# Kernel tuning notes

Hardware: AMD Instinct MI355X
Metric: run time of the kernel (lower is better)

The kernel has to match this reference:

```python
import jax, jax.numpy as jnp
import numpy as np

OUT_FEATURES = 11008  # LLaMA-7B FFN intermediate
IN_FEATURES = 4096    # d_model
N_TOKENS = 16         # small M -> weight-traffic bound
SCALE = 0.01
ZERO_POINT = 0


def setup_inputs() -> dict:
    key = jax.random.key(0)
    k1, k2 = jax.random.split(key)
    x = jax.random.normal(k1, (N_TOKENS, IN_FEATURES), dtype=jnp.float32)
    weight_int8 = jax.random.randint(
        k2, (OUT_FEATURES, IN_FEATURES), -128, 128, dtype=jnp.int32
    ).astype(jnp.int8)
    return {
        "x": x,
        "weight_int8": weight_int8,
        "scale": SCALE,
        "zero_point": ZERO_POINT,
    }


def reference(x, weight_int8, scale, zero_point):
    # Dequantize INT8 weight to fp32 (same elementwise pass as the torch module)
    weight_fp = (weight_int8.astype(jnp.float32) - zero_point) * scale  # [out, in]
    # F.linear(x, W) == x @ W.T
    return jnp.einsum("ti,oi->to", x, weight_fp)
```

## Files before the change

kernel.cpp:

```cpp
#include <hip/hip_runtime.h>
#include <hip/hip_bf16.h>
#include <stdint.h>


#define M_TOK 16
#define K_DIM 4096
#define N_OUT 11008

typedef int v4i __attribute__((ext_vector_type(4)));

__global__ __launch_bounds__(256) void quant_x_kernel(
    const float* __restrict__ x, int8_t* __restrict__ xh,
    int8_t* __restrict__ xl, float* __restrict__ s1_out,
    float* __restrict__ sumx_out) {
  const int t = blockIdx.x;
  const int tid = threadIdx.x;
  const float4* xv = (const float4*)(x + (long)t * K_DIM) + tid * 4;

  float vals[16];
  float m = 0.0f, s = 0.0f;
#pragma unroll
  for (int j = 0; j < 4; ++j) {
    float4 f = xv[j];
    vals[j * 4 + 0] = f.x; vals[j * 4 + 1] = f.y;
    vals[j * 4 + 2] = f.z; vals[j * 4 + 3] = f.w;
    m = fmaxf(m, fmaxf(fmaxf(fabsf(f.x), fabsf(f.y)),
                       fmaxf(fabsf(f.z), fabsf(f.w))));
    s += f.x + f.y + f.z + f.w;
  }
#pragma unroll
  for (int off = 32; off > 0; off >>= 1) {
    m = fmaxf(m, __shfl_xor(m, off));
    s += __shfl_xor(s, off);
  }
  __shared__ float lm[4], ls[4];
  const int w = tid >> 6;
  if ((tid & 63) == 0) { lm[w] = m; ls[w] = s; }
  __syncthreads();
  m = fmaxf(fmaxf(lm[0], lm[1]), fmaxf(lm[2], lm[3]));
  s = ls[0] + ls[1] + ls[2] + ls[3];

  const float s1 = (m > 0.0f) ? (m * (1.0f / 127.0f)) : 1.0f;
  const float inv = 1.0f / s1;
  if (tid == 0) { s1_out[t] = s1; sumx_out[t] = s; }

  int hq[16], lq[16];
#pragma unroll
  for (int j = 0; j < 16; ++j) {
    float xf = vals[j];
    float h = rintf(xf * inv);
    h = fminf(fmaxf(h, -127.0f), 127.0f);
    float resid = xf - h * s1;
    float l = rintf(resid * inv * 256.0f);
    l = fminf(fmaxf(l, -128.0f), 127.0f);
    hq[j] = (int)h;
    lq[j] = (int)l;
  }
  int4 hv, lv;
  int* hp = (int*)&hv;
  int* lp = (int*)&lv;
#pragma unroll
  for (int d = 0; d < 4; ++d) {
    uint32_t hw = 0, lw = 0;
#pragma unroll
    for (int j = 0; j < 4; ++j) {
      hw |= (uint32_t)(hq[d * 4 + j] & 0xff) << (8 * j);
      lw |= (uint32_t)(lq[d * 4 + j] & 0xff) << (8 * j);
    }
    hp[d] = (int)hw;
    lp[d] = (int)lw;
  }
  ((int4*)xh)[(long)t * 256 + tid] = hv;
  ((int4*)xl)[(long)t * 256 + tid] = lv;
}

__global__ __launch_bounds__(256) void qgemm_kernel(
    const int* __restrict__ W, const int8_t* __restrict__ xh,
    const int8_t* __restrict__ xl, const float* __restrict__ s1,
    const float* __restrict__ sumx, const float* __restrict__ scale_p,
    const int* __restrict__ zp_p, float* __restrict__ out) {
  const int tid = threadIdx.x;
  const int lane = tid & 63;
  const int w = tid >> 6;
  const int obase = blockIdx.x * 16;
  const int n = lane & 15;
  const int g = lane >> 4;
  const long kbase = (long)w * 1024 + g * 16;

  const int* Wp = W + (long)(obase + n) * K_DIM + kbase;
  const v4i* Ah = (const v4i*)(xh + (long)n * K_DIM + kbase);
  const v4i* Al = (const v4i*)(xl + (long)n * K_DIM + kbase);

  v4i accH = {0, 0, 0, 0};
  v4i accL = {0, 0, 0, 0};
#pragma unroll 4
  for (int c = 0; c < 16; ++c) {
    const int4* wq = (const int4*)(Wp + c * 64);
    v4i b;
#pragma unroll
    for (int d = 0; d < 4; ++d) {
      int4 q = wq[d];
      uint32_t packed = ((uint32_t)q.x & 0xffu) |
                        (((uint32_t)q.y & 0xffu) << 8) |
                        (((uint32_t)q.z & 0xffu) << 16) |
                        (((uint32_t)q.w & 0xffu) << 24);
      b[d] = (int)packed;
    }
    v4i ah = Ah[c * 4];
    v4i al = Al[c * 4];
    accH = __builtin_amdgcn_mfma_i32_16x16x64_i8(ah, b, accH, 0, 0, 0);
    accL = __builtin_amdgcn_mfma_i32_16x16x64_i8(al, b, accL, 0, 0, 0);
  }

  __shared__ float red[4][16 * 17];
#pragma unroll
  for (int r = 0; r < 4; ++r) {
    float f = (float)accH[r] + (float)accL[r] * (1.0f / 256.0f);
    int t = g * 4 + r;
    red[w][t * 17 + n] = f;
  }
  __syncthreads();

  const int t = tid >> 4;
  const int col = tid & 15;
  float sum = red[0][t * 17 + col] + red[1][t * 17 + col] +
              red[2][t * 17 + col] + red[3][t * 17 + col];
  const float sc = scale_p[0];
  const float zp = (float)zp_p[0];
  float o = sc * (s1[t] * sum) - sc * zp * sumx[t];
  out[(long)t * N_OUT + obase + col] = o;
}

extern "C" void kernel_launch(void* const* d_in, const int* in_sizes, int n_in,
                              void* d_out, int out_size, void* d_ws,
                              size_t ws_size, hipStream_t stream) {
  const float* x = (const float*)d_in[0];
  const int* Wq = (const int*)d_in[1];
  const float* scale_p = (const float*)d_in[2];
  const int* zp_p = (const int*)d_in[3];
  float* out = (float*)d_out;

  int8_t* xh = (int8_t*)d_ws;
  int8_t* xl = xh + (long)M_TOK * K_DIM;
  float* s1 = (float*)(xl + (long)M_TOK * K_DIM);
  float* sumx = s1 + M_TOK;

  quant_x_kernel<<<M_TOK, 256, 0, stream>>>(x, xh, xl, s1, sumx);
  qgemm_kernel<<<N_OUT / 16, 256, 0, stream>>>(Wq, xh, xl, s1, sumx, scale_p,
                                               zp_p, out);
}
```

Baseline: 255.1 us.

## Double-buffer weight tiles via async global-to-LDS loads with swizzled layout

The GEMM kernel now streams weight tiles into shared memory with `global_load_lds` DMA, double-buffered so the next stage's load is in flight while MFMAs run on the current one. The K split across waves is reorganised so each wave owns 64-int slices per stage. Lanes now read 256 contiguous bytes per row instead of 64, which should coalesce better. An XOR swizzle is meant to avoid LDS bank conflicts on readback. The code relies on the compiler inserting vmcnt waits before the LDS reads and adds no explicit barrier, which is a correctness risk; LDS use also grows, which may lower occupancy.

```diff
diff --git a/kernel.cpp b/kernel.cpp
--- a/kernel.cpp
+++ b/kernel.cpp
@@ -8,6 +8,11 @@
 #define N_OUT 11008
 
 typedef int v4i __attribute__((ext_vector_type(4)));
+
+#define GLOAD_LDS16(g, l)                                               \
+  __builtin_amdgcn_global_load_lds(                                     \
+      (const __attribute__((address_space(1))) void*)(g),               \
+      (__attribute__((address_space(3))) void*)(l), 16, 0, 0)
 
 __global__ __launch_bounds__(256) void quant_x_kernel(
     const float* __restrict__ x, int8_t* __restrict__ xh,
@@ -85,31 +90,61 @@
   const int obase = blockIdx.x * 16;
   const int n = lane & 15;
   const int g = lane >> 4;
-  const long kbase = (long)w * 1024 + g * 16;
 
-  const int* Wp = W + (long)(obase + n) * K_DIM + kbase;
-  const v4i* Ah = (const v4i*)(xh + (long)n * K_DIM + kbase);
-  const v4i* Al = (const v4i*)(xl + (long)n * K_DIM + kbase);
+  __shared__ int wlds[2][4][1024];
+
+  const int* gj0 = W + (long)(obase + 0 + g) * K_DIM + w * 64 + ((n ^ g) ^ 0) * 4;
+  const int* gj1 = W + (long)(obase + 4 + g) * K_DIM + w * 64 + ((n ^ g) ^ 4) * 4;
+  const int* gj2 = W + (long)(obase + 8 + g) * K_DIM + w * 64 + ((n ^ g) ^ 0) * 4;
+  const int* gj3 = W + (long)(obase + 12 + g) * K_DIM + w * 64 + ((n ^ g) ^ 4) * 4;
+
+  const int Q0 = (g * 4) ^ (n & 7);
+  const int r0 = n * 64 + ((Q0 ^ 0)) * 4;
+  const int r1 = n * 64 + ((Q0 ^ 1)) * 4;
+  const int r2 = n * 64 + ((Q0 ^ 2)) * 4;
+  const int r3 = n * 64 + ((Q0 ^ 3)) * 4;
+
+  const v4i* Ah = (const v4i*)(xh + (long)n * K_DIM + w * 64 + g * 16);
+  const v4i* Al = (const v4i*)(xl + (long)n * K_DIM + w * 64 + g * 16);
 
   v4i accH = {0, 0, 0, 0};
   v4i accL = {0, 0, 0, 0};
-#pragma unroll 4
-  for (int c = 0; c < 16; ++c) {
-    const int4* wq = (const int4*)(Wp + c * 64);
-    v4i b;
+
+  GLOAD_LDS16(gj0, &wlds[0][w][0]);
+  GLOAD_LDS16(gj1, &wlds[0][w][256]);
+  GLOAD_LDS16(gj2, &wlds[0][w][512]);
+  GLOAD_LDS16(gj3, &wlds[0][w][768]);
+
 #pragma unroll
-    for (int d = 0; d < 4; ++d) {
-      int4 q = wq[d];
-      uint32_t packed = ((uint32_t)q.x & 0xffu) |
-                        (((uint32_t)q.y & 0xffu) << 8) |
-                        (((uint32_t)q.z & 0xffu) << 16) |
-                        (((uint32_t)q.w & 0xffu) << 24);
-      b[d] = (int)packed;
+  for (int s = 0; s < 16; ++s) {
+    const int b = s & 1;
+    if (s + 1 < 16) {
+      const int soff = (s + 1) * 256;
+      GLOAD_LDS16(gj0 + soff, &wlds[b ^ 1][w][0]);
+      GLOAD_LDS16(gj1 + soff, &wlds[b ^ 1][w][256]);
+      GLOAD_LDS16(gj2 + soff, &wlds[b ^ 1][w][512]);
+      GLOAD_LDS16(gj3 + soff, &wlds[b ^ 1][w][768]);
     }
-    v4i ah = Ah[c * 4];
-    v4i al = Al[c * 4];
-    accH = __builtin_amdgcn_mfma_i32_16x16x64_i8(ah, b, accH, 0, 0, 0);
-    accL = __builtin_amdgcn_mfma_i32_16x16x64_i8(al, b, accL, 0, 0, 0);
+    v4i ah = Ah[s * 16];
+    v4i al = Al[s * 16];
+
+    v4i q0 = *(const v4i*)&wlds[b][w][r0];
+    v4i q1 = *(const v4i*)&wlds[b][w][r1];
+    v4i q2 = *(const v4i*)&wlds[b][w][r2];
+    v4i q3 = *(const v4i*)&wlds[b][w][r3];
+
+    v4i bf;
+    bf[0] = (int)(((uint32_t)q0[0] & 0xffu) | (((uint32_t)q0[1] & 0xffu) << 8) |
+                  (((uint32_t)q0[2] & 0xffu) << 16) | ((uint32_t)q0[3] << 24));
+    bf[1] = (int)(((uint32_t)q1[0] & 0xffu) | (((uint32_t)q1[1] & 0xffu) << 8) |
+                  (((uint32_t)q1[2] & 0xffu) << 16) | ((uint32_t)q1[3] << 24));
+    bf[2] = (int)(((uint32_t)q2[0] & 0xffu) | (((uint32_t)q2[1] & 0xffu) << 8) |
+                  (((uint32_t)q2[2] & 0xffu) << 16) | ((uint32_t)q2[3] << 24));
+    bf[3] = (int)(((uint32_t)q3[0] & 0xffu) | (((uint32_t)q3[1] & 0xffu) << 8) |
+                  (((uint32_t)q3[2] & 0xffu) << 16) | ((uint32_t)q3[3] << 24));
+
+    accH = __builtin_amdgcn_mfma_i32_16x16x64_i8(ah, bf, accH, 0, 0, 0);
+    accL = __builtin_amdgcn_mfma_i32_16x16x64_i8(al, bf, accL, 0, 0, 0);
   }
 
   __shared__ float red[4][16 * 17];
```

Measured after the change: 256.5 us. No clear change (+0.5%).
